# Kernel tuning notes

Hardware: AMD Instinct MI355X
Metric: run time of the kernel (lower is better)

The kernel has to match this reference:

```python
import jax, jax.numpy as jnp
import numpy as np

DIM_EMB = 1024
TIMESTEP = 4096
BATCH = 16


def _make_pe(timestep: int, dim_emb: int) -> jnp.ndarray:
    # Faithful to the source's (nonstandard) indexing:
    #   pe[pos, i]   = sin(pos / 10000**(2*i/D))       for even i
    #   pe[pos, i+1] = cos(pos / 10000**(2*(i+1)/D))
    pos = jnp.arange(timestep, dtype=jnp.float32)[:, None]          # [T, 1]
    i_even = jnp.arange(0, dim_emb, 2, dtype=jnp.float32)           # [D/2]
    div_sin = jnp.power(10000.0, 2.0 * i_even / dim_emb)            # [D/2]
    div_cos = jnp.power(10000.0, 2.0 * (i_even + 1.0) / dim_emb)    # [D/2]
    pe = jnp.zeros((timestep, dim_emb), dtype=jnp.float32)
    pe = pe.at[:, 0::2].set(jnp.sin(pos / div_sin))
    pe = pe.at[:, 1::2].set(jnp.cos(pos / div_cos))
    return pe


def setup_inputs() -> dict:
    key = jax.random.key(0)
    x = jax.random.normal(key, (BATCH, TIMESTEP, DIM_EMB), dtype=jnp.float32)
    return {"x": x}


def reference(x) -> jnp.ndarray:
    B, T, D = x.shape
    pe = _make_pe(TIMESTEP, D)[:T]                 # [T, D]
    # dropout p=0.0 (eval / identity)
    return x * jnp.sqrt(jnp.float32(D)) + pe[None, :, :]
```

## Files before the change

kernel.cpp:

```cpp
#include <hip/hip_runtime.h>
#include <math.h>

#define DIM_EMB 1024
#define TIMESTEP 4096
#define BATCH 16


typedef float f4 __attribute__((ext_vector_type(4)));

__global__ __launch_bounds__(256)
void Pos_embedding_39161511805397_kernel(const float* __restrict__ x,
                                         float* __restrict__ out) {
    const int t   = blockIdx.x;
    const int tid = threadIdx.x;
    const int c0  = tid << 2;

    const float pos = (float)t;
    const float k = -13.287712379549449f / 512.0f;
    const float a0 = pos * exp2f(k * (float)(c0 + 0));
    const float a1 = pos * exp2f(k * (float)(c0 + 1));
    const float a2 = pos * exp2f(k * (float)(c0 + 2));
    const float a3 = pos * exp2f(k * (float)(c0 + 3));

    f4 pe;
    pe.x = sinf(a0);
    pe.y = cosf(a1);
    pe.z = sinf(a2);
    pe.w = cosf(a3);

    const float s = 32.0f;

    const f4* __restrict__ xv = (const f4*)x;
    f4* __restrict__ ov       = (f4*)out;

    const size_t base   = ((size_t)t * DIM_EMB + (size_t)c0) >> 2;
    const size_t stride = ((size_t)TIMESTEP * DIM_EMB) >> 2;

    f4 v[BATCH];
    #pragma unroll
    for (int b = 0; b < BATCH; ++b) {
        v[b] = __builtin_nontemporal_load(xv + base + (size_t)b * stride);
    }

    #pragma unroll
    for (int b = 0; b < BATCH; ++b) {
        f4 r;
        r.x = fmaf(v[b].x, s, pe.x);
        r.y = fmaf(v[b].y, s, pe.y);
        r.z = fmaf(v[b].z, s, pe.z);
        r.w = fmaf(v[b].w, s, pe.w);
        __builtin_nontemporal_store(r, ov + base + (size_t)b * stride);
    }
}

extern "C" void kernel_launch(void* const* d_in, const int* in_sizes, int n_in,
                              void* d_out, int out_size, void* d_ws, size_t ws_size,
                              hipStream_t stream) {
    const float* x = (const float*)d_in[0];
    float* out     = (float*)d_out;
    dim3 grid(TIMESTEP);
    dim3 block(256);
    Pos_embedding_39161511805397_kernel<<<grid, block, 0, stream>>>(x, out);
}
```

Baseline: 439.9 us.

## Flatten grid to one float4 per thread and use hardware sin/cos

Replaces the per-timestep blocks, which loaded all 16 batch rows into registers, with a flat grid where each thread handles one float4 and recomputes the positional encoding itself. Sine and cosine now go through range reduction plus the AMD hardware sin/cos instructions instead of libm sinf/cosf. This trades 16x redundant PE computation for much higher parallelism and lower register pressure on a memory-bound streaming kernel. The hardware sin/cos with large arguments (pos up to 4095) may lose accuracy compared with the reference.

```diff
diff --git a/kernel.cpp b/kernel.cpp
--- a/kernel.cpp
+++ b/kernel.cpp
@@ -8,49 +8,54 @@
 
 typedef float f4 __attribute__((ext_vector_type(4)));
 
+__device__ __forceinline__ float fast_sin(float a) {
+    const float INV2PI = 0.15915494309189535f;
+    float r = a * INV2PI;
+    r = r - rintf(r);
+    return __builtin_amdgcn_sinf(r);
+}
+
+__device__ __forceinline__ float fast_cos(float a) {
+    const float INV2PI = 0.15915494309189535f;
+    float r = a * INV2PI;
+    r = r - rintf(r);
+    return __builtin_amdgcn_cosf(r);
+}
+
 __global__ __launch_bounds__(256)
 void Pos_embedding_39161511805397_kernel(const float* __restrict__ x,
                                          float* __restrict__ out) {
-    const int t   = blockIdx.x;
-    const int tid = threadIdx.x;
-    const int c0  = tid << 2;
-
-    const float pos = (float)t;
-    const float k = -13.287712379549449f / 512.0f;
-    const float a0 = pos * exp2f(k * (float)(c0 + 0));
-    const float a1 = pos * exp2f(k * (float)(c0 + 1));
-    const float a2 = pos * exp2f(k * (float)(c0 + 2));
-    const float a3 = pos * exp2f(k * (float)(c0 + 3));
-
-    f4 pe;
-    pe.x = sinf(a0);
-    pe.y = cosf(a1);
-    pe.z = sinf(a2);
-    pe.w = cosf(a3);
-
-    const float s = 32.0f;
+    const int g = blockIdx.x * 256 + threadIdx.x;
+    const int c4 = g & (DIM_EMB / 4 - 1);
+    const int t  = (g >> 8) & (TIMESTEP - 1);
+    const int c0 = c4 << 2;
 
     const f4* __restrict__ xv = (const f4*)x;
     f4* __restrict__ ov       = (f4*)out;
 
-    const size_t base   = ((size_t)t * DIM_EMB + (size_t)c0) >> 2;
-    const size_t stride = ((size_t)TIMESTEP * DIM_EMB) >> 2;
+    f4 v = __builtin_nontemporal_load(xv + g);
 
-    f4 v[BATCH];
-    #pragma unroll
-    for (int b = 0; b < BATCH; ++b) {
-        v[b] = __builtin_nontemporal_load(xv + base + (size_t)b * stride);
-    }
+    const float pos = (float)t;
+    const float k  = -13.287712379549449f / 512.0f;
+    const float e0 = k * (float)c0;
+    const float a0 = pos * exp2f(e0);
+    const float a1 = pos * exp2f(e0 + k);
+    const float a2 = pos * exp2f(e0 + 2.0f * k);
+    const float a3 = pos * exp2f(e0 + 3.0f * k);
 
-    #pragma unroll
-    for (int b = 0; b < BATCH; ++b) {
-        f4 r;
-        r.x = fmaf(v[b].x, s, pe.x);
-        r.y = fmaf(v[b].y, s, pe.y);
-        r.z = fmaf(v[b].z, s, pe.z);
-        r.w = fmaf(v[b].w, s, pe.w);
-        __builtin_nontemporal_store(r, ov + base + (size_t)b * stride);
-    }
+    f4 pe;
+    pe.x = fast_sin(a0);
+    pe.y = fast_cos(a1);
+    pe.z = fast_sin(a2);
+    pe.w = fast_cos(a3);
+
+    const float s = 32.0f;
+    f4 r;
+    r.x = fmaf(v.x, s, pe.x);
+    r.y = fmaf(v.y, s, pe.y);
+    r.z = fmaf(v.z, s, pe.z);
+    r.w = fmaf(v.w, s, pe.w);
+    __builtin_nontemporal_store(r, ov + g);
 }
 
 extern "C" void kernel_launch(void* const* d_in, const int* in_sizes, int n_in,
@@ -58,7 +63,8 @@
                               hipStream_t stream) {
     const float* x = (const float*)d_in[0];
     float* out     = (float*)d_out;
-    dim3 grid(TIMESTEP);
+    const int total_f4 = BATCH * TIMESTEP * (DIM_EMB / 4);
+    dim3 grid(total_f4 / 256);
     dim3 block(256);
     Pos_embedding_39161511805397_kernel<<<grid, block, 0, stream>>>(x, out);
 }
```

Measured after the change: 408.8 us. -7.1%, faster.
